# Kernel tuning notes

Hardware: AMD Instinct MI355X
Metric: run time of the kernel (lower is better)

## Reference

```python
import jax, jax.numpy as jnp
import numpy as np

LEAKY_SLOPE = 0.2
NEG_INF = -9e15
LN_EPS = 1e-5


def conv1x1(x, W, b):
    # x: [B, Cin, N, L], W: [Cout, Cin], b: [Cout] -> [B, Cout, N, L]
    return jnp.einsum('bcnl,oc->bonl', x, W) + b[None, :, None, None]


def gat_layer(h, mask, W, a, concat):
    # h: [B, L, N, Fin], mask: [N, N] bool, W: [Fin, Fout], a: [2*Fout, 1]
    Wh = h @ W                                   # [B, L, N, Fout]
    F_out = W.shape[1]
    Wh1 = Wh @ a[:F_out]                         # [B, L, N, 1]
    Wh2 = Wh @ a[F_out:]                         # [B, L, N, 1]
    e = jax.nn.leaky_relu(Wh1 + jnp.swapaxes(Wh2, -1, -2), LEAKY_SLOPE)  # [B,L,N,N]
    att = jnp.where(mask, e, NEG_INF)
    att = jax.nn.softmax(att, axis=-1)
    h_prime = att @ Wh                           # [B, L, N, Fout]
    return jax.nn.elu(h_prime) if concat else h_prime


def custom_layernorm(x):
    # normalizes over dims (1, 2) as in the torch LayerNorm (affine disabled)
    m = x.mean(axis=(1, 2), keepdims=True)
    v = x.var(axis=(1, 2), keepdims=True)
    return (x - m) / jnp.sqrt(v + LN_EPS)


def setup_inputs() -> dict:
    key = jax.random.key(0)
    ks = jax.random.split(key, 16)
    B, C, N, L = 4, 256, 1024, 12
    s = 0.06  # ~xavier scale for 256-dim fans
    return {
        'x_in': jax.random.normal(ks[0], (B, C, N, L), dtype=jnp.float32),
        'D_Graph': jax.random.randint(ks[1], (N, N), 0, 2, dtype=jnp.int32),
        'nodevec1': jax.random.normal(ks[2], (N, 6), dtype=jnp.float32),
        'nodevec2': jax.random.normal(ks[3], (6, N), dtype=jnp.float32),
        'W_mlp': jax.random.normal(ks[4], (C, 2 * C), dtype=jnp.float32) * 0.04,
        'b_mlp': jnp.zeros((C,), dtype=jnp.float32),
        'W_g0': jax.random.normal(ks[5], (C, C), dtype=jnp.float32) * s,
        'a_g0': jax.random.normal(ks[6], (2 * C, 1), dtype=jnp.float32) * s,
        'W_go': jax.random.normal(ks[7], (C, C), dtype=jnp.float32) * s,
        'a_go': jax.random.normal(ks[8], (2 * C, 1), dtype=jnp.float32) * s,
        'Wg1': jax.random.normal(ks[9], (C, C), dtype=jnp.float32) * s,
        'bg1': jnp.zeros((C,), dtype=jnp.float32),
        'Wg2': jax.random.normal(ks[10], (C, C), dtype=jnp.float32) * s,
        'bg2': jnp.zeros((C,), dtype=jnp.float32),
        'Wg3': jax.random.normal(ks[11], (C, C), dtype=jnp.float32) * s,
        'bg3': jnp.zeros((C,), dtype=jnp.float32),
        'alpha': jnp.float32(-5.0),
        'weight': jnp.ones((C, N, 1), dtype=jnp.float32),
        'bias': jnp.zeros((C, N, 1), dtype=jnp.float32),
    }


def reference(x_in, D_Graph, nodevec1, nodevec2, W_mlp, b_mlp, W_g0, a_g0,
              W_go, a_go, Wg1, bg1, Wg2, bg2, Wg3, bg3, alpha, weight, bias):
    # --- adaptive-adjacency GCN branch (support_len=1, order=1) ---
    adp = jax.nn.softmax(jax.nn.relu(nodevec1 @ nodevec2), axis=1)  # [N, N]
    x1 = jnp.einsum('bcvl,wv->bcwl', x_in, adp)
    h = jnp.concatenate([x_in, x1], axis=1)                         # [B, 2C, N, L]
    x_gcn = conv1x1(h, W_mlp, b_mlp)                                # [B, C, N, L]

    # --- dense adjacency-masked GAT branch (nheads=1, order=1) ---
    mask = D_Graph > 0
    ht = jnp.transpose(x_in, (0, 3, 2, 1))                          # [B, L, N, C]
    g = gat_layer(ht, mask, W_g0, a_g0, concat=True)
    g = jax.nn.elu(gat_layer(g, mask, W_go, a_go, concat=False))
    x_gat = jnp.transpose(g, (0, 3, 2, 1))                          # [B, C, N, L]

    # --- fuse, residual, norm, GLU, affine ---
    a_s = jax.nn.sigmoid(alpha)
    x = a_s * x_gat + (1.0 - a_s) * x_gcn + x_in
    x = custom_layernorm(x)
    g1 = conv1x1(x, Wg1, bg1)
    g2 = conv1x1(x, Wg2, bg2)
    glu_out = conv1x1(g1 * jax.nn.sigmoid(g2), Wg3, bg3)
    x = glu_out + x
    x = x * weight[None] + bias[None] + x
    x = custom_layernorm(x)
    return x
```

## Files before the change

### kernel.cpp

```cpp
#include <hip/hip_runtime.h>
#include <hip/hip_bf16.h>
#include <math.h>

#define DI __device__ __forceinline__
#define AS1 __attribute__((address_space(1)))
#define AS3 __attribute__((address_space(3)))

static constexpr int  B_ = 4, C_ = 256, N_ = 1024, L_ = 12, BL_ = 48;
static constexpr long SLAB = (long)N_ * C_;
static constexpr long TOT  = (long)BL_ * SLAB;

typedef __attribute__((ext_vector_type(8))) short bf16x8;
typedef __attribute__((ext_vector_type(4))) float f32x4;
typedef __attribute__((ext_vector_type(4))) uint u32x4;

DI float b2f(uint hw) { return __builtin_bit_cast(float, (hw & 0xffffu) << 16); }
DI ushort f2b(float f) {
    uint u = __builtin_bit_cast(uint, f);
    u += 0x7FFFu + ((u >> 16) & 1u);
    return (ushort)(u >> 16);
}
DI uint pack2(float a, float b) {
    __hip_bfloat162 h = __float22bfloat162_rn(make_float2(a, b));
    uint r;
    __builtin_memcpy(&r, &h, 4);
    return r;
}
DI float fexp2(float x) {
#if __has_builtin(__builtin_amdgcn_exp2f)
    return __builtin_amdgcn_exp2f(x);
#else
    return __expf(x * 0.6931471805599453f);
#endif
}

DI void gload16(const void* g, void* l) {
    __builtin_amdgcn_global_load_lds((AS1 uint*)g, (AS3 uint*)l, 16, 0, 0);
}

DI float block_sum256(float v, float* sc) {
    #pragma unroll
    for (int o = 32; o > 0; o >>= 1) v += __shfl_xor(v, o, 64);
    int wid = threadIdx.x >> 6;
    __syncthreads();
    if ((threadIdx.x & 63) == 0) sc[wid] = v;
    __syncthreads();
    return sc[0] + sc[1] + sc[2] + sc[3];
}
DI float block_max256(float v, float* sc) {
    #pragma unroll
    for (int o = 32; o > 0; o >>= 1) v = fmaxf(v, __shfl_xor(v, o, 64));
    int wid = threadIdx.x >> 6;
    __syncthreads();
    if ((threadIdx.x & 63) == 0) sc[wid] = v;
    __syncthreads();
    return fmaxf(fmaxf(sc[0], sc[1]), fmaxf(sc[2], sc[3]));
}

__global__ __launch_bounds__(256) void k_adp(const float* __restrict__ nv1,
                                             const float* __restrict__ nv2,
                                             ushort* __restrict__ adp) {
    __shared__ float r[6];
    __shared__ float sc[4];
    int row = blockIdx.x, tid = threadIdx.x;
    if (tid < 6) r[tid] = nv1[row * 6 + tid];
    __syncthreads();
    float e[4];
    #pragma unroll
    for (int q = 0; q < 4; q++) {
        int j = tid + q * 256;
        float s = 0.f;
        #pragma unroll
        for (int k = 0; k < 6; k++) s += r[k] * nv2[k * 1024 + j];
        e[q] = s > 0.f ? s : 0.f;
    }
    float m = fmaxf(fmaxf(e[0], e[1]), fmaxf(e[2], e[3]));
    m = block_max256(m, sc);
    float ps = 0.f;
    #pragma unroll
    for (int q = 0; q < 4; q++) { e[q] = __expf(e[q] - m); ps += e[q]; }
    ps = block_sum256(ps, sc);
    float rinv = 1.f / ps;
    #pragma unroll
    for (int q = 0; q < 4; q++) adp[(long)row * 1024 + tid + q * 256] = f2b(e[q] * rinv);
}

__global__ __launch_bounds__(256) void k_tin(const float* __restrict__ x,
                                             ushort* __restrict__ xb,
                                             float* __restrict__ xf) {
    __shared__ float t[64][65];
    int nl0 = blockIdx.x * 64, c0 = blockIdx.y * 64, b = blockIdx.z;
    int lx = threadIdx.x & 63, ly = threadIdx.x >> 6;
    #pragma unroll
    for (int i = 0; i < 16; i++) {
        int c = c0 + ly + i * 4;
        t[ly + i * 4][lx] = x[(long)(b * 256 + c) * 12288 + nl0 + lx];
    }
    __syncthreads();
    #pragma unroll
    for (int i = 0; i < 16; i++) {
        int nl = nl0 + ly + i * 4;
        int n = nl / 12, l = nl % 12;
        long idx = ((long)(b * 12 + l) * 1024 + n) * 256 + c0 + lx;
        float v = t[lx][ly + i * 4];
        xb[idx] = f2b(v);
        xf[idx] = v;
    }
}

__global__ __launch_bounds__(256) void k_xtt(const ushort* __restrict__ X,
                                             ushort* __restrict__ XT) {
    __shared__ ushort t[64][68];
    int bl = blockIdx.z;
    int n0 = blockIdx.x * 64, c0 = blockIdx.y * 64;
    int lx = threadIdx.x & 63, ly = threadIdx.x >> 6;
    const ushort* Xp = X + (long)bl * SLAB;
    #pragma unroll
    for (int i = 0; i < 16; i++)
        t[ly + i * 4][lx] = Xp[(long)(n0 + ly + i * 4) * 256 + c0 + lx];
    __syncthreads();
    ushort* Tp = XT + (long)bl * SLAB;
    #pragma unroll
    for (int i = 0; i < 16; i++)
        Tp[(long)(c0 + ly + i * 4) * 1024 + n0 + lx] = t[lx][ly + i * 4];
}

__global__ __launch_bounds__(256) void k_wt2(const float* __restrict__ S0, ushort* __restrict__ D0,
                                             const float* __restrict__ S1, ushort* __restrict__ D1) {
    __shared__ float t[64][65];
    const float* S = blockIdx.z ? S1 : S0;
    ushort* D = blockIdx.z ? D1 : D0;
    int c0 = blockIdx.x * 64, o0 = blockIdx.y * 64;
    int lx = threadIdx.x & 63, ly = threadIdx.x >> 6;
    #pragma unroll
    for (int i = 0; i < 16; i++)
        t[ly + i * 4][lx] = S[(long)(c0 + ly + i * 4) * 256 + o0 + lx];
    __syncthreads();
    #pragma unroll
    for (int i = 0; i < 16; i++)
        D[(long)(o0 + ly + i * 4) * 256 + c0 + lx] = f2b(t[lx][ly + i * 4]);
}

__global__ __launch_bounds__(256) void k_wconv(const float* __restrict__ S, ushort* __restrict__ D) {
    long i = (long)blockIdx.x * 256 + threadIdx.x;
    D[i] = f2b(S[i]);
}

__global__ __launch_bounds__(256) void k_wgi(const float* __restrict__ W1, const float* __restrict__ b1,
                                             const float* __restrict__ W2, const float* __restrict__ b2,
                                             ushort* __restrict__ WGI, float* __restrict__ BI) {
    int n = blockIdx.x, p = n >> 5, q = n & 31;
    const float* src = (q < 16) ? W1 + (long)(p * 16 + q) * 256
                                : W2 + (long)(p * 16 + q - 16) * 256;
    WGI[(long)n * 256 + threadIdx.x] = f2b(src[threadIdx.x]);
    if (threadIdx.x == 0) BI[n] = (q < 16) ? b1[p * 16 + q] : b2[p * 16 + q - 16];
}

__global__ __launch_bounds__(256) void k_va(const float* __restrict__ W, const float* __restrict__ a,
                                            float* __restrict__ va) {
    __shared__ float sc[4];
    int c = blockIdx.x, t = threadIdx.x;
    float w = W[(long)c * 256 + t];
    float s1 = block_sum256(w * a[t], sc);
    float s2 = block_sum256(w * a[256 + t], sc);
    if (t == 0) { va[c] = s1; va[256 + c] = s2; }
}

__global__ __launch_bounds__(256) void k_wtprep(const float* __restrict__ w,
                                                const float* __restrict__ b,
                                                float* __restrict__ wt,
                                                float* __restrict__ bt) {
    int n = blockIdx.x, c = threadIdx.x;
    wt[(long)n * 256 + c] = w[(long)c * 1024 + n] + 1.f;
    bt[(long)n * 256 + c] = b[(long)c * 1024 + n];
}

__global__ __launch_bounds__(256) void k_maskpack(const int* __restrict__ dg,
                                                  uint* __restrict__ maskw) {
    int w = blockIdx.x * 256 + threadIdx.x;
    int row = w >> 5, wo = w & 31;
    uint m = 0;
    #pragma unroll
    for (int b = 0; b < 32; b++)
        m |= (dg[(long)row * 1024 + wo * 32 + b] > 0 ? 1u : 0u) << b;
    maskw[w] = m;
}

template<int NPAIR, int GLU>
__global__ __launch_bounds__(256) void k_bgemm(
    const ushort* __restrict__ A0, long sA0,
    const ushort* __restrict__ A1, long sA1,
    int lda, int K0, int KK,
    const ushort* __restrict__ Bt, long sBt,
    const float* __restrict__ bias,
    float* __restrict__ Cf, ushort* __restrict__ Cb, long sC,
    const float* __restrict__ biasi,
    const float* __restrict__ FA, const float2* __restrict__ ST1,
    const float* __restrict__ WTp, const float* __restrict__ BTp,
    float2* __restrict__ partOut) {
    __shared__ ushort As[2][128 * 32];
    __shared__ ushort Bs[2][128 * 32];
    __shared__ float sc[4];
    const int tid = threadIdx.x;
    const int bl = blockIdx.z;
    const int m0 = blockIdx.x * 128, n0 = blockIdx.y * 128;
    const int N = gridDim.y * 128;
    const int lane = tid & 63, w = tid >> 6;
    const int wm = (w >> 1) * 64, wn = (w & 1) * 64;
    const int sr = tid >> 2, sk = (tid & 3) * 8;
    const int fr = lane & 15, fk = (lane >> 4) * 8;
    f32x4 acc[4][4] = {};
    const ushort* Ab0 = A0 + (long)bl * sA0;
    const ushort* Ab1 = (NPAIR == 2) ? A1 + (long)bl * sA1 : nullptr;
    const ushort* Bb = Bt + (long)bl * sBt;

    auto stage = [&](int buf, int k0) {
        const ushort* Asrc = Ab0; int kl = k0;
        if (NPAIR == 2 && k0 >= K0) { Asrc = Ab1; kl = k0 - K0; }
        gload16(&Asrc[(long)(m0 + sr) * lda + kl + sk],      &As[buf][sr * 32 + sk]);
        gload16(&Asrc[(long)(m0 + sr + 64) * lda + kl + sk], &As[buf][(sr + 64) * 32 + sk]);
        gload16(&Bb[(long)(n0 + sr) * KK + k0 + sk],         &Bs[buf][sr * 32 + sk]);
        gload16(&Bb[(long)(n0 + sr + 64) * KK + k0 + sk],    &Bs[buf][(sr + 64) * 32 + sk]);
    };
    auto compute = [&](int buf) {
        bf16x8 af[4], bg[4];
        #pragma unroll
        for (int i = 0; i < 4; i++) {
            af[i] = *(const bf16x8*)&As[buf][(wm + i * 16 + fr) * 32 + fk];
            bg[i] = *(const bf16x8*)&Bs[buf][(wn + i * 16 + fr) * 32 + fk];
        }
        #pragma unroll
        for (int i = 0; i < 4; i++)
            #pragma unroll
            for (int j = 0; j < 4; j++)
                acc[i][j] = __builtin_amdgcn_mfma_f32_16x16x32_bf16(af[i], bg[j], acc[i][j], 0, 0, 0);
    };

    stage(0, 0);
    __syncthreads();
    int cur = 0;
    for (int k0 = 32; k0 < KK; k0 += 32) {
        stage(cur ^ 1, k0);
        compute(cur);
        __syncthreads();
        cur ^= 1;
    }
    compute(cur);

    const int cn = lane & 15, rb = (lane >> 4) * 4;
    if (GLU == 1) {
        #pragma unroll
        for (int nt = 0; nt < 4; nt += 2) {
            int n1 = n0 + wn + nt * 16 + cn;
            int hcol = ((n1 >> 5) << 4) + cn;
            float b1 = biasi[n1], b2 = biasi[n1 + 16];
            #pragma unroll
            for (int i = 0; i < 4; i++) {
                #pragma unroll
                for (int r = 0; r < 4; r++) {
                    int m = m0 + wm + i * 16 + rb + r;
                    float g1 = acc[i][nt][r] + b1;
                    float g2 = acc[i][nt + 1][r] + b2;
                    float h = g1 / (1.f + __expf(-g2));
                    Cb[(long)bl * sC + (long)m * 256 + hcol] = f2b(h);
                }
            }
        }
    } else if (GLU == 2) {
        float2 st = ST1[bl];
        float ssum = 0.f, qsum = 0.f;
        #pragma unroll
        for (int j = 0; j < 4; j++) {
            int n = n0 + wn + j * 16 + cn;
            float bv = bias[n];
            #pragma unroll
            for (int i = 0; i < 4; i++) {
                #pragma unroll
                for (int r = 0; r < 4; r++) {
                    int m = m0 + wm + i * 16 + rb + r;
                    long idx = (long)bl * sC + (long)m * N + n;
                    float xn = (FA[idx] - st.x) * st.y;
                    float v = (acc[i][j][r] + bv + xn) * WTp[m * 256 + n] + BTp[m * 256 + n];
                    Cf[idx] = v;
                    ssum += v;
                    qsum += v * v;
                }
            }
        }
        ssum = block_sum256(ssum, sc);
        qsum = block_sum256(qsum, sc);
        if (tid == 0)
            partOut[bl * 16 + blockIdx.x * 2 + blockIdx.y] = make_float2(ssum, qsum);
    } else {
        #pragma unroll
        for (int j = 0; j < 4; j++) {
            int n = n0 + wn + j * 16 + cn;
            float bv = bias ? bias[n] : 0.f;
            #pragma unroll
            for (int i = 0; i < 4; i++) {
                #pragma unroll
                for (int r = 0; r < 4; r++) {
                    int m = m0 + wm + i * 16 + rb + r;
                    float v = acc[i][j][r] + bv;
                    long idx = (long)bl * sC + (long)m * N + n;
                    if (Cf) Cf[idx] = v;
                    if (Cb) Cb[idx] = f2b(v);
                }
            }
        }
    }
}

__global__ __launch_bounds__(256) void k_dots(const ushort* __restrict__ X,
                                              const float* __restrict__ va,
                                              float* __restrict__ o1,
                                              float* __restrict__ o2) {
    int wid = threadIdx.x >> 6, lane = threadIdx.x & 63;
    long row = (long)blockIdx.x * 4 + wid;
    uint2 xv = *(const uint2*)(X + row * 256 + lane * 4);
    float x0 = b2f(xv.x), x1 = b2f(xv.x >> 16), x2 = b2f(xv.y), x3 = b2f(xv.y >> 16);
    float4 v1 = *(const float4*)&va[lane * 4];
    float4 v2 = *(const float4*)&va[256 + lane * 4];
    float s1 = x0 * v1.x + x1 * v1.y + x2 * v1.z + x3 * v1.w;
    float s2 = x0 * v2.x + x1 * v2.y + x2 * v2.z + x3 * v2.w;
    #pragma unroll
    for (int o = 32; o > 0; o >>= 1) { s1 += __shfl_xor(s1, o, 64); s2 += __shfl_xor(s2, o, 64); }
    if (lane == 0) { o1[row] = s1; o2[row] = s2; }
}

__global__ __launch_bounds__(256) void k_w2max(const float* __restrict__ w2v,
                                               float* __restrict__ w2m) {
    __shared__ float sc[4];
    int bl = blockIdx.x;
    float4 v = *(const float4*)&w2v[(long)bl * 1024 + threadIdx.x * 4];
    float m = fmaxf(fmaxf(v.x, v.y), fmaxf(v.z, v.w));
    m = block_max256(m, sc);
    if (threadIdx.x == 0) w2m[bl] = m;
}

template<int FUSE>
__global__ __launch_bounds__(256, 3) void k_attn_mf(
    const ushort* __restrict__ WhT,
    const float* __restrict__ w1v, const float* __restrict__ w2v,
    const float* __restrict__ w2m,
    const uint* __restrict__ maskw,
    ushort* __restrict__ outB,
    const float* __restrict__ gcn, const float* __restrict__ xf,
    const float* __restrict__ alpha,
    float* __restrict__ outF, float2* __restrict__ part) {
    __shared__ float w2E[1024];
    __shared__ float w2F[1024];
    __shared__ uint msk[64 * 33];
    __shared__ uint mlut[4];
    __shared__ float sc[4];
    constexpr float LOG2E = 1.4426950408889634f;
    int d = blockIdx.x;
    int lidx = (d & 7) * 96 + (d >> 3);
    int bl = lidx >> 4;
    int i0 = (lidx & 15) * 64;
    int tid = threadIdx.x;
    #pragma unroll
    for (int q = 0; q < 4; q++) {
        float v = w2v[(long)bl * 1024 + tid + q * 256];
        w2E[tid + q * 256] = fexp2(v * LOG2E);
        w2F[tid + q * 256] = fexp2(v * (0.2f * LOG2E));
    }
    if (tid < 4) mlut[tid] = ((tid & 1) ? 0x0000FFFFu : 0u) | ((tid & 2) ? 0xFFFF0000u : 0u);
    {
        const uint4* gm = (const uint4*)(maskw + (long)i0 * 32);
        uint4 ma = gm[tid * 2], mb = gm[tid * 2 + 1];
        int r0 = tid >> 2, w0 = (tid & 3) * 8;
        uint* mp = &msk[r0 * 33 + w0];
        mp[0] = ma.x; mp[1] = ma.y; mp[2] = ma.z; mp[3] = ma.w;
        mp[4] = mb.x; mp[5] = mb.y; mp[6] = mb.z; mp[7] = mb.w;
    }
    __syncthreads();
    const int lane = tid & 63, w = tid >> 6;
    const int wn = w * 64;
    const int fr = lane & 15, fg = lane >> 4, fk8 = fg * 8;
    const float w2mL = w2m[bl] * LOG2E;
    float c1[4], c2[4];
    #pragma unroll
    for (int mt = 0; mt < 4; mt++) {
        float w1L = w1v[(long)bl * 1024 + i0 + mt * 16 + fr] * LOG2E;
        float e0 = w1L + w2mL;
        float mrL = fmaxf(e0, 0.2f * e0);
        c1[mt] = fexp2(w1L - mrL);
        c2[mt] = fexp2(0.2f * w1L - mrL);
    }
    f32x4 acc[4][4] = {};
    f32x4 acc_s[4] = {};
    u32x4 ov; ov[0] = ov[1] = ov[2] = ov[3] = 0x3F803F80u;
    const bf16x8 onesf = __builtin_bit_cast(bf16x8, ov);
    const ushort* bp = WhT + (long)bl * SLAB;
    #pragma unroll 1
    for (int ks = 0; ks < 32; ks++) {
        bf16x8 bg[4];
        #pragma unroll
        for (int nt = 0; nt < 4; nt++)
            bg[nt] = *(const bf16x8*)&bp[(long)(wn + nt * 16 + fr) * 1024 + ks * 32 + fk8];
        float4 ea = *(const float4*)&w2E[ks * 32 + fk8];
        float4 eb = *(const float4*)&w2E[ks * 32 + fk8 + 4];
        float4 fa = *(const float4*)&w2F[ks * 32 + fk8];
        float4 fb = *(const float4*)&w2F[ks * 32 + fk8 + 4];
        #pragma unroll
        for (int mt = 0; mt < 4; mt++) {
            uint mby = (msk[(mt * 16 + fr) * 33 + ks] >> (fg * 8)) & 0xffu;
            float p0 = fmaxf(c1[mt] * ea.x, c2[mt] * fa.x);
            float p1 = fmaxf(c1[mt] * ea.y, c2[mt] * fa.y);
            float p2 = fmaxf(c1[mt] * ea.z, c2[mt] * fa.z);
            float p3 = fmaxf(c1[mt] * ea.w, c2[mt] * fa.w);
            float p4 = fmaxf(c1[mt] * eb.x, c2[mt] * fb.x);
            float p5 = fmaxf(c1[mt] * eb.y, c2[mt] * fb.y);
            float p6 = fmaxf(c1[mt] * eb.z, c2[mt] * fb.z);
            float p7 = fmaxf(c1[mt] * eb.w, c2[mt] * fb.w);
            u32x4 av;
            av[0] = pack2(p0, p1) & mlut[mby & 3];
            av[1] = pack2(p2, p3) & mlut[(mby >> 2) & 3];
            av[2] = pack2(p4, p5) & mlut[(mby >> 4) & 3];
            av[3] = pack2(p6, p7) & mlut[(mby >> 6) & 3];
            bf16x8 af = __builtin_bit_cast(bf16x8, av);
            acc_s[mt] = __builtin_amdgcn_mfma_f32_16x16x32_bf16(af, onesf, acc_s[mt], 0, 0, 0);
            #pragma unroll
            for (int nt = 0; nt < 4; nt++)
                acc[mt][nt] = __builtin_amdgcn_mfma_f32_16x16x32_bf16(
                    af, bg[nt], acc[mt][nt], 0, 0, 0);
        }
    }
    float as = 0.f, bs = 0.f, ssum = 0.f, qsum = 0.f;
    if (FUSE) { as = 1.f / (1.f + __expf(-alpha[0])); bs = 1.f - as; }
    #pragma unroll
    for (int mt = 0; mt < 4; mt++) {
        #pragma unroll
        for (int r = 0; r < 4; r++) {
            float si = 1.f / acc_s[mt][r];
            int i = mt * 16 + fg * 4 + r;
            #pragma unroll
            for (int nt = 0; nt < 4; nt++) {
                int c = wn + nt * 16 + fr;
                float v = acc[mt][nt][r] * si;
                v = (v > 0.f) ? v : __expf(v) - 1.f;
                long idx = (long)bl * SLAB + (long)(i0 + i) * 256 + c;
                if (FUSE) {
                    float fv = as * v + bs * gcn[idx] + xf[idx];
                    outF[idx] = fv;
                    ssum += fv;
                    qsum += fv * fv;
                } else {
                    outB[idx] = f2b(v);
                }
            }
        }
    }
    if (FUSE) {
        ssum = block_sum256(ssum, sc);
        qsum = block_sum256(qsum, sc);
        if (tid == 0) part[bl * 16 + (lidx & 15)] = make_float2(ssum, qsum);
    }
}

__global__ void k_stats16(const float2* __restrict__ part, float2* __restrict__ stats) {
    int bl = blockIdx.x, t = threadIdx.x;
    float s = 0.f, q = 0.f;
    if (t < 16) { float2 v = part[bl * 16 + t]; s = v.x; q = v.y; }
    #pragma unroll
    for (int o = 8; o > 0; o >>= 1) { s += __shfl_xor(s, o, 64); q += __shfl_xor(q, o, 64); }
    if (t == 0) {
        float mean = s / (float)SLAB;
        float var = q / (float)SLAB - mean * mean;
        stats[bl] = make_float2(mean, 1.f / sqrtf(var + 1e-5f));
    }
}

__global__ __launch_bounds__(256) void k_ln_apply(const float4* __restrict__ x,
                                                  const float2* __restrict__ stats,
                                                  ushort* __restrict__ ob) {
    long i = (long)blockIdx.x * 256 + threadIdx.x;
    int bl = (int)(i >> 16);
    float2 st = stats[bl];
    float4 v = x[i];
    uint2 ow;
    ow.x = pack2((v.x - st.x) * st.y, (v.y - st.x) * st.y);
    ow.y = pack2((v.z - st.x) * st.y, (v.w - st.x) * st.y);
    ((uint2*)ob)[i] = ow;
}

__global__ __launch_bounds__(256) void k_out(const float* __restrict__ x,
                                             const float2* __restrict__ stats,
                                             float* __restrict__ out) {
    int n = blockIdx.x, b = blockIdx.y, c = threadIdx.x;
    float v[12];
    #pragma unroll
    for (int l = 0; l < 12; l++) {
        float2 st = stats[b * 12 + l];
        float t = x[(long)(b * 12 + l) * SLAB + (long)n * 256 + c];
        v[l] = (t - st.x) * st.y;
    }
    float4* op = (float4*)(out + ((long)(b * 256 + c) * 1024 + n) * 12);
    op[0] = make_float4(v[0], v[1], v[2], v[3]);
    op[1] = make_float4(v[4], v[5], v[6], v[7]);
    op[2] = make_float4(v[8], v[9], v[10], v[11]);
}

extern "C" void kernel_launch(void* const* d_in, const int* in_sizes, int n_in,
                              void* d_out, int out_size, void* d_ws, size_t ws_size,
                              hipStream_t stream) {
    (void)in_sizes; (void)n_in; (void)out_size; (void)ws_size;
    const float* x_in = (const float*)d_in[0];
    const int*   dg   = (const int*)d_in[1];
    const float* nv1  = (const float*)d_in[2];
    const float* nv2  = (const float*)d_in[3];
    const float* Wmlp = (const float*)d_in[4];
    const float* bmlp = (const float*)d_in[5];
    const float* Wg0  = (const float*)d_in[6];
    const float* ag0  = (const float*)d_in[7];
    const float* Wgo  = (const float*)d_in[8];
    const float* ago  = (const float*)d_in[9];
    const float* Wg1  = (const float*)d_in[10];
    const float* bg1  = (const float*)d_in[11];
    const float* Wg2  = (const float*)d_in[12];
    const float* bg2  = (const float*)d_in[13];
    const float* Wg3  = (const float*)d_in[14];
    const float* bg3  = (const float*)d_in[15];
    const float* alpha = (const float*)d_in[16];
    const float* wgt  = (const float*)d_in[17];
    const float* bia  = (const float*)d_in[18];
    float* out = (float*)d_out;

    float* XTf = (float*)d_ws;
    float* Bf  = XTf + TOT;
    ushort* U1 = (ushort*)(Bf + TOT);
    ushort* U2 = U1 + TOT;
    float* Af  = (float*)U1;
    ushort* U3 = U2 + TOT;
    ushort* U4 = U3 + TOT;
    ushort* ADPB = U4 + TOT;
    ushort* WMLPB = ADPB + (long)1024 * 1024;
    ushort* WG0T = WMLPB + 131072;
    ushort* WGOT = WG0T + 65536;
    ushort* WGIB = WGOT + 65536;
    ushort* WG3B = WGIB + 131072;
    float* BIASI = (float*)(WG3B + 65536);
    float* VA = BIASI + 512;
    float* W1V = VA + 1024;
    float* W2V = W1V + 49152;
    float* W2M = W2V + 49152;
    uint* MASKW = (uint*)(W2M + 64);
    float2* PART = (float2*)(MASKW + 32768);
    float2* STATS1 = PART + 48 * 16;
    float2* STATS2 = STATS1 + 48;
    float* WT = (float*)(STATS2 + 48);
    float* BT2 = WT + SLAB;

    dim3 blk(256);
    k_wt2<<<dim3(4, 4, 2), blk, 0, stream>>>(Wg0, WG0T, Wgo, WGOT);
    k_wconv<<<512, blk, 0, stream>>>(Wmlp, WMLPB);
    k_wconv<<<256, blk, 0, stream>>>(Wg3, WG3B);
    k_wgi<<<512, blk, 0, stream>>>(Wg1, bg1, Wg2, bg2, WGIB, BIASI);
    k_va<<<256, blk, 0, stream>>>(Wg0, ag0, VA);
    k_va<<<256, blk, 0, stream>>>(Wgo, ago, VA + 512);
    k_wtprep<<<1024, blk, 0, stream>>>(wgt, bia, WT, BT2);
    k_adp<<<1024, blk, 0, stream>>>(nv1, nv2, ADPB);
    k_maskpack<<<128, blk, 0, stream>>>(dg, MASKW);
    k_tin<<<dim3(192, 4, 4), blk, 0, stream>>>(x_in, U1, XTf);
    k_xtt<<<dim3(16, 4, 48), blk, 0, stream>>>(U1, U2);
    k_bgemm<1, 0><<<dim3(8, 2, 48), blk, 0, stream>>>(ADPB, 0, nullptr, 0, 1024, 0, 1024,
        U2, SLAB, nullptr, nullptr, U3, SLAB, nullptr,
        nullptr, nullptr, nullptr, nullptr, nullptr);
    k_bgemm<2, 0><<<dim3(8, 2, 48), blk, 0, stream>>>(U1, SLAB, U3, SLAB, 256, 256, 512,
        WMLPB, 0, bmlp, Bf, nullptr, SLAB, nullptr,
        nullptr, nullptr, nullptr, nullptr, nullptr);
    k_dots<<<12288, blk, 0, stream>>>(U1, VA, W1V, W2V);
    k_w2max<<<48, blk, 0, stream>>>(W2V, W2M);
    k_bgemm<1, 0><<<dim3(2, 8, 48), blk, 0, stream>>>(WG0T, 0, nullptr, 0, 256, 0, 256,
        U1, SLAB, nullptr, nullptr, U4, SLAB, nullptr,
        nullptr, nullptr, nullptr, nullptr, nullptr);
    k_attn_mf<0><<<768, blk, 0, stream>>>(U4, W1V, W2V, W2M, MASKW, U2,
                                          nullptr, nullptr, nullptr, nullptr, nullptr);
    k_dots<<<12288, blk, 0, stream>>>(U2, VA + 512, W1V, W2V);
    k_w2max<<<48, blk, 0, stream>>>(W2V, W2M);
    k_bgemm<1, 0><<<dim3(2, 8, 48), blk, 0, stream>>>(WGOT, 0, nullptr, 0, 256, 0, 256,
        U2, SLAB, nullptr, nullptr, U4, SLAB, nullptr,
        nullptr, nullptr, nullptr, nullptr, nullptr);
    k_attn_mf<1><<<768, blk, 0, stream>>>(U4, W1V, W2V, W2M, MASKW, nullptr,
                                          Bf, XTf, alpha, Af, PART);
    k_stats16<<<48, 64, 0, stream>>>(PART, STATS1);
    k_ln_apply<<<12288, blk, 0, stream>>>((const float4*)Af, STATS1, U3);
    k_bgemm<1, 1><<<dim3(8, 4, 48), blk, 0, stream>>>(U3, SLAB, nullptr, 0, 256, 0, 256,
        WGIB, 0, nullptr, nullptr, U4, SLAB, BIASI,
        nullptr, nullptr, nullptr, nullptr, nullptr);
    k_bgemm<1, 2><<<dim3(8, 2, 48), blk, 0, stream>>>(U4, SLAB, nullptr, 0, 256, 0, 256,
        WG3B, 0, bg3, Bf, nullptr, SLAB, nullptr,
        Af, STATS1, WT, BT2, PART);
    k_stats16<<<48, 64, 0, stream>>>(PART, STATS2);
    k_out<<<dim3(1024, 4), blk, 0, stream>>>(Bf, STATS2, out);
}
```

Measured before the change: 484.0 us.

## Share attention probability tiles across waves via double-buffered LDS

Before, every wave recomputed the masked exp probabilities for all 64 rows, so the exp/pack work was duplicated four times across the block's waves. Now each thread computes one row's probabilities for a 32-column slice, writes them into a double-buffered shared P tile, and all waves read that tile as MFMA A-operands, with the next chunk computed while MFMAs run on the current one. This removes the redundant VALU work at the cost of 32KB more LDS, extra block barriers and LDS round-trips, which may lower occupancy at the 3-blocks-per-CU launch bound.

```diff
diff --git a/kernel.cpp b/kernel.cpp
--- a/kernel.cpp
+++ b/kernel.cpp
@@ -348,6 +348,8 @@
     const float* __restrict__ gcn, const float* __restrict__ xf,
     const float* __restrict__ alpha,
     float* __restrict__ outF, float2* __restrict__ part) {
+    __shared__ ushort PA[16 * 64 * 8];
+    __shared__ ushort PB[16 * 64 * 8];
     __shared__ float w2E[1024];
     __shared__ float w2F[1024];
     __shared__ uint msk[64 * 33];
@@ -376,57 +378,102 @@
     }
     __syncthreads();
     const int lane = tid & 63, w = tid >> 6;
+    const int row = lane, jt = w;
     const int wn = w * 64;
     const int fr = lane & 15, fg = lane >> 4, fk8 = fg * 8;
     const float w2mL = w2m[bl] * LOG2E;
-    float c1[4], c2[4];
-    #pragma unroll
-    for (int mt = 0; mt < 4; mt++) {
-        float w1L = w1v[(long)bl * 1024 + i0 + mt * 16 + fr] * LOG2E;
+    float c1r, c2r;
+    {
+        float w1L = w1v[(long)bl * 1024 + i0 + row] * LOG2E;
         float e0 = w1L + w2mL;
         float mrL = fmaxf(e0, 0.2f * e0);
-        c1[mt] = fexp2(w1L - mrL);
-        c2[mt] = fexp2(0.2f * w1L - mrL);
+        c1r = fexp2(w1L - mrL);
+        c2r = fexp2(0.2f * w1L - mrL);
     }
     f32x4 acc[4][4] = {};
     f32x4 acc_s[4] = {};
     u32x4 ov; ov[0] = ov[1] = ov[2] = ov[3] = 0x3F803F80u;
     const bf16x8 onesf = __builtin_bit_cast(bf16x8, ov);
     const ushort* bp = WhT + (long)bl * SLAB;
+
+    auto computeP = [&](int jc, ushort* Pb) {
+        uint mw = msk[row * 33 + jc * 4 + jt];
+        #pragma unroll
+        for (int u = 0; u < 4; u++) {
+            uint mby = (mw >> (u * 8)) & 0xffu;
+            int jb = jc * 128 + jt * 32 + u * 8;
+            float4 ea = *(const float4*)&w2E[jb];
+            float4 eb = *(const float4*)&w2E[jb + 4];
+            float4 fa = *(const float4*)&w2F[jb];
+            float4 fb = *(const float4*)&w2F[jb + 4];
+            float p0 = fmaxf(c1r * ea.x, c2r * fa.x);
+            float p1 = fmaxf(c1r * ea.y, c2r * fa.y);
+            float p2 = fmaxf(c1r * ea.z, c2r * fa.z);
+            float p3 = fmaxf(c1r * ea.w, c2r * fa.w);
+            float p4 = fmaxf(c1r * eb.x, c2r * fb.x);
+            float p5 = fmaxf(c1r * eb.y, c2r * fb.y);
+            float p6 = fmaxf(c1r * eb.z, c2r * fb.z);
+            float p7 = fmaxf(c1r * eb.w, c2r * fb.w);
+            u32x4 pv;
+            pv[0] = pack2(p0, p1) & mlut[mby & 3];
+            pv[1] = pack2(p2, p3) & mlut[(mby >> 2) & 3];
+            pv[2] = pack2(p4, p5) & mlut[(mby >> 4) & 3];
+            pv[3] = pack2(p6, p7) & mlut[(mby >> 6) & 3];
+            *(u32x4*)((char*)Pb + ((jt * 4 + u) * 64 + row) * 16) = pv;
+        }
+    };
+    auto mfmaC = [&](int jc, const ushort* Pb) {
+        #pragma unroll
+        for (int ks = 0; ks < 4; ks++) {
+            int kb = jc * 128 + ks * 32 + fk8;
+            bf16x8 bg0 = *(const bf16x8*)&bp[(long)(wn + 0 * 16 + fr) * 1024 + kb];
+            bf16x8 bg1 = *(const bf16x8*)&bp[(long)(wn + 1 * 16 + fr) * 1024 + kb];
+            bf16x8 bg2 = *(const bf16x8*)&bp[(long)(wn + 2 * 16 + fr) * 1024 + kb];
+            bf16x8 bg3 = *(const bf16x8*)&bp[(long)(wn + 3 * 16 + fr) * 1024 + kb];
+            int kq = ks * 4 + fg;
+            bf16x8 af0 = *(const bf16x8*)((const char*)Pb + (kq * 64 + 0 * 16 + fr) * 16);
+            bf16x8 af1 = *(const bf16x8*)((const char*)Pb + (kq * 64 + 1 * 16 + fr) * 16);
+            bf16x8 af2 = *(const bf16x8*)((const char*)Pb + (kq * 64 + 2 * 16 + fr) * 16);
+            bf16x8 af3 = *(const bf16x8*)((const char*)Pb + (kq * 64 + 3 * 16 + fr) * 16);
+            acc_s[0] = __builtin_amdgcn_mfma_f32_16x16x32_bf16(af0, onesf, acc_s[0], 0, 0, 0);
+            acc_s[1] = __builtin_amdgcn_mfma_f32_16x16x32_bf16(af1, onesf, acc_s[1], 0, 0, 0);
+            acc_s[2] = __builtin_amdgcn_mfma_f32_16x16x32_bf16(af2, onesf, acc_s[2], 0, 0, 0);
+            acc_s[3] = __builtin_amdgcn_mfma_f32_16x16x32_bf16(af3, onesf, acc_s[3], 0, 0, 0);
+            acc[0][0] = __builtin_amdgcn_mfma_f32_16x16x32_bf16(af0, bg0, acc[0][0], 0, 0, 0);
+            acc[0][1] = __builtin_amdgcn_mfma_f32_16x16x32_bf16(af0, bg1, acc[0][1], 0, 0, 0);
+            acc[0][2] = __builtin_amdgcn_mfma_f32_16x16x32_bf16(af0, bg2, acc[0][2], 0, 0, 0);
+            acc[0][3] = __builtin_amdgcn_mfma_f32_16x16x32_bf16(af0, bg3, acc[0][3], 0, 0, 0);
+            acc[1][0] = __builtin_amdgcn_mfma_f32_16x16x32_bf16(af1, bg0, acc[1][0], 0, 0, 0);
+            acc[1][1] = __builtin_amdgcn_mfma_f32_16x16x32_bf16(af1, bg1, acc[1][1], 0, 0, 0);
+            acc[1][2] = __builtin_amdgcn_mfma_f32_16x16x32_bf16(af1, bg2, acc[1][2], 0, 0, 0);
+            acc[1][3] = __builtin_amdgcn_mfma_f32_16x16x32_bf16(af1, bg3, acc[1][3], 0, 0, 0);
+            acc[2][0] = __builtin_amdgcn_mfma_f32_16x16x32_bf16(af2, bg0, acc[2][0], 0, 0, 0);
+            acc[2][1] = __builtin_amdgcn_mfma_f32_16x16x32_bf16(af2, bg1, acc[2][1], 0, 0, 0);
+            acc[2][2] = __builtin_amdgcn_mfma_f32_16x16x32_bf16(af2, bg2, acc[2][2], 0, 0, 0);
+            acc[2][3] = __builtin_amdgcn_mfma_f32_16x16x32_bf16(af2, bg3, acc[2][3], 0, 0, 0);
+            acc[3][0] = __builtin_amdgcn_mfma_f32_16x16x32_bf16(af3, bg0, acc[3][0], 0, 0, 0);
+            acc[3][1] = __builtin_amdgcn_mfma_f32_16x16x32_bf16(af3, bg1, acc[3][1], 0, 0, 0);
+            acc[3][2] = __builtin_amdgcn_mfma_f32_16x16x32_bf16(af3, bg2, acc[3][2], 0, 0, 0);
+            acc[3][3] = __builtin_amdgcn_mfma_f32_16x16x32_bf16(af3, bg3, acc[3][3], 0, 0, 0);
+        }
+    };
+
+    computeP(0, PA);
+    __syncthreads();
     #pragma unroll 1
-    for (int ks = 0; ks < 32; ks++) {
-        bf16x8 bg[4];
-        #pragma unroll
-        for (int nt = 0; nt < 4; nt++)
-            bg[nt] = *(const bf16x8*)&bp[(long)(wn + nt * 16 + fr) * 1024 + ks * 32 + fk8];
-        float4 ea = *(const float4*)&w2E[ks * 32 + fk8];
-        float4 eb = *(const float4*)&w2E[ks * 32 + fk8 + 4];
-        float4 fa = *(const float4*)&w2F[ks * 32 + fk8];
-        float4 fb = *(const float4*)&w2F[ks * 32 + fk8 + 4];
-        #pragma unroll
-        for (int mt = 0; mt < 4; mt++) {
-            uint mby = (msk[(mt * 16 + fr) * 33 + ks] >> (fg * 8)) & 0xffu;
-            float p0 = fmaxf(c1[mt] * ea.x, c2[mt] * fa.x);
-            float p1 = fmaxf(c1[mt] * ea.y, c2[mt] * fa.y);
-            float p2 = fmaxf(c1[mt] * ea.z, c2[mt] * fa.z);
-            float p3 = fmaxf(c1[mt] * ea.w, c2[mt] * fa.w);
-            float p4 = fmaxf(c1[mt] * eb.x, c2[mt] * fb.x);
-            float p5 = fmaxf(c1[mt] * eb.y, c2[mt] * fb.y);
-            float p6 = fmaxf(c1[mt] * eb.z, c2[mt] * fb.z);
-            float p7 = fmaxf(c1[mt] * eb.w, c2[mt] * fb.w);
-            u32x4 av;
-            av[0] = pack2(p0, p1) & mlut[mby & 3];
-            av[1] = pack2(p2, p3) & mlut[(mby >> 2) & 3];
-            av[2] = pack2(p4, p5) & mlut[(mby >> 4) & 3];
-            av[3] = pack2(p6, p7) & mlut[(mby >> 6) & 3];
-            bf16x8 af = __builtin_bit_cast(bf16x8, av);
-            acc_s[mt] = __builtin_amdgcn_mfma_f32_16x16x32_bf16(af, onesf, acc_s[mt], 0, 0, 0);
-            #pragma unroll
-            for (int nt = 0; nt < 4; nt++)
-                acc[mt][nt] = __builtin_amdgcn_mfma_f32_16x16x32_bf16(
-                    af, bg[nt], acc[mt][nt], 0, 0, 0);
-        }
-    }
+    for (int jc = 0; jc < 6; jc += 2) {
+        computeP(jc + 1, PB);
+        mfmaC(jc, PA);
+        __syncthreads();
+        computeP(jc + 2, PA);
+        mfmaC(jc + 1, PB);
+        __syncthreads();
+    }
+    computeP(7, PB);
+    mfmaC(6, PA);
+    __syncthreads();
+    mfmaC(7, PB);
+
     float as = 0.f, bs = 0.f, ssum = 0.f, qsum = 0.f;
     if (FUSE) { as = 1.f / (1.f + __expf(-alpha[0])); bs = 1.f - as; }
     #pragma unroll
```

Measured after the change: 608.0 us. 25.6% more time.
